# Optimization experiments

Measured on AMD Instinct MI355X. Metric: run time of the kernel, lower is better.

The kernel has to match this reference:

```python
import jax, jax.numpy as jnp
import numpy as np

N, E, B = 30000, 360000, 8
FN, FE, D, L, M = 64, 16, 128, 3, 8
DK = D // M
NEG_SLOPE = 0.2
EPS = 1e-5


def setup_inputs() -> dict:
    key = jax.random.key(0)
    ks = jax.random.split(key, 24)
    rng = np.random.default_rng(0)
    Ng, Eg = N // B, E // B
    off = np.repeat(np.arange(B, dtype=np.int64) * Ng, Eg)
    src = jnp.asarray(rng.integers(0, Ng, size=E) + off, dtype=jnp.int32)
    dst = jnp.asarray(rng.integers(0, Ng, size=E) + off, dtype=jnp.int32)
    node_graph = jnp.asarray(np.repeat(np.arange(B), Ng), dtype=jnp.int32)
    edge_graph = jnp.asarray(np.repeat(np.arange(B), Eg), dtype=jnp.int32)
    p = lambda i, *s: jax.random.normal(ks[i], s, jnp.float32) * 0.05
    return dict(
        h=jax.random.normal(ks[0], (N, FN), jnp.float32),
        e=jax.random.normal(ks[1], (E, FE), jnp.float32),
        src=src, dst=dst, node_graph=node_graph, edge_graph=edge_graph,
        emb_n_w=p(2, D, FN), emb_n_b=p(3, D),
        emb_e_w=p(4, D, FE), emb_e_b=p(5, D),
        Us=p(6, L, D, D), Vs=p(7, L, D, D), As=p(8, L, D, D),
        Bs=p(9, L, D, D), Cs=p(10, L, D, D),
        gat_src_w=p(11, M * DK, D), gat_src_b=p(12, M * DK),
        gat_dst_w=p(13, M * DK, D), gat_dst_b=p(14, M * DK),
        gat_attn=p(15, M, DK), gat_bias=p(16, M * DK),
        O_w=p(17, D, D), O_b=p(18, D),
        W1_w=p(19, D, 3 * D), W1_b=p(20, D),
        W2_w=p(21, 1, D), W2_b=p(22, 1))


def _bn(x):
    # BatchNorm1d(affine=False), training mode: biased variance over batch dim
    return (x - x.mean(0)) * jax.lax.rsqrt(x.var(0) + EPS)


def reference(h, e, src, dst, node_graph, edge_graph,
              emb_n_w, emb_n_b, emb_e_w, emb_e_b,
              Us, Vs, As, Bs, Cs,
              gat_src_w, gat_src_b, gat_dst_w, gat_dst_b, gat_attn, gat_bias,
              O_w, O_b, W1_w, W1_b, W2_w, W2_b):
    h = h @ emb_n_w.T + emb_n_b  # [N, D]
    e = e @ emb_e_w.T + emb_e_b  # [E, D]
    for l in range(L):
        # u_mul_e('h','w','m') + max('m','agg'): gather-mul-segment_max
        m = (h @ Vs[l].T)[src] * jax.nn.sigmoid(e)  # [E, D]
        agg = jax.ops.segment_max(m, dst, num_segments=N)
        agg = jnp.where(jnp.isneginf(agg), 0.0, agg)  # DGL fills zero-in-degree with 0
        h_new = h + jax.nn.relu(_bn(h @ Us[l].T + agg))
        # inc('in')^T @ B(h) = B(h)[dst]; inc('out')^T @ C(h) = C(h)[src] (uses pre-update h)
        ee = (h @ Bs[l].T)[dst] + (h @ Cs[l].T)[src]
        e = e + jax.nn.relu(_bn(e @ As[l].T + ee))
        h = h_new
    # GATv2Conv(D, DK, M heads, allow_zero_in_degree=True)
    fs = (h @ gat_src_w.T + gat_src_b).reshape(N, M, DK)
    fd = (h @ gat_dst_w.T + gat_dst_b).reshape(N, M, DK)
    z = jax.nn.leaky_relu(fs[src] + fd[dst], NEG_SLOPE)  # [E, M, DK]
    score = jnp.einsum('emk,mk->em', z, gat_attn)        # [E, M]
    smax = jax.ops.segment_max(score, dst, num_segments=N)[dst]
    p = jnp.exp(score - smax)
    denom = jax.ops.segment_sum(p, dst, num_segments=N)[dst]
    a = p / denom
    rst = jax.ops.segment_sum(a[:, :, None] * fs[src], dst, num_segments=N)
    rst = rst + gat_bias.reshape(1, M, DK)
    h = rst.reshape(N, D) @ O_w.T + O_b
    # per-graph mean of node states, broadcast to that graph's edges
    cnt = jax.ops.segment_sum(jnp.ones((N,), h.dtype), node_graph, num_segments=B)
    moy = jax.ops.segment_sum(h, node_graph, num_segments=B) / cnt[:, None]
    out = jnp.concatenate([moy[edge_graph], h[src], h[dst]], axis=1)  # [E, 3D]
    out = jax.nn.relu(out @ W1_w.T + W1_b)
    out = out @ W2_w.T + W2_b
    return jax.nn.sigmoid(out)[:, 0]
```

## Files before the change

kernel.cpp:

```cpp
#include <hip/hip_runtime.h>

#define DF 128
#define NGRAPH 8

typedef __attribute__((ext_vector_type(8))) short bf16x8;
typedef __attribute__((ext_vector_type(4))) float f32x4;

__device__ __forceinline__ float sigm(float x) { return 1.f / (1.f + __expf(-x)); }
__device__ __forceinline__ unsigned short f2bf(float f) {
  unsigned u = __float_as_uint(f);
  u += 0x7FFFu + ((u >> 16) & 1u);
  return (unsigned short)(u >> 16);
}
__device__ __forceinline__ float bf2f(unsigned short u) {
  return __uint_as_float(((unsigned)u) << 16);
}
__device__ __forceinline__ float bflo(unsigned u) { return __uint_as_float(u << 16); }
__device__ __forceinline__ float bfhi(unsigned u) { return __uint_as_float(u & 0xffff0000u); }

__device__ __forceinline__ bf16x8 cvt8(const float* __restrict__ p) {
  float4 a = *(const float4*)p;
  float4 b = *(const float4*)(p + 4);
  bf16x8 r;
  r[0] = (short)f2bf(a.x); r[1] = (short)f2bf(a.y);
// ... 119 lines not shown
  for (int i = tid; i < 16 * DF; i += 128) Wt[(i & 15) * DF + (i >> 4)] = w[i];
  float bb = b[tid];
  __syncthreads();
  for (int r0 = blockIdx.x * 4; r0 < rows; r0 += gridDim.x * 4) {
    if (tid < 64) ar[tid >> 4][tid & 15] = ein[(size_t)r0 * 16 + tid];
    __syncthreads();
    float a0 = bb, a1 = bb, a2 = bb, a3 = bb;
#pragma unroll
    for (int k = 0; k < 16; ++k) {
      float wv = Wt[k * DF + tid];
      a0 = fmaf(ar[0][k], wv, a0); a1 = fmaf(ar[1][k], wv, a1);
      a2 = fmaf(ar[2][k], wv, a2); a3 = fmaf(ar[3][k], wv, a3);
    }
    e0u[(size_t)r0 * DF + tid] = f2bf(a0);
    e0u[(size_t)(r0 + 1) * DF + tid] = f2bf(a1);
    e0u[(size_t)(r0 + 2) * DF + tid] = f2bf(a2);
    e0u[(size_t)(r0 + 3) * DF + tid] = f2bf(a3);
    __syncthreads();
  }
}

template <int OUTBF>
__global__ __launch_bounds__(512) void k_gemm_mfma(
    const float* __restrict__ A, const short* __restrict__ Wf,
    const float* __restrict__ bias, void* __restrict__ outv, int rows) {
  __shared__ short Wb[2048 * 8];
  int tid = threadIdx.x;
  for (int s = tid; s < 2048; s += 512)
    *(bf16x8*)&Wb[s * 8] = *(const bf16x8*)&Wf[(size_t)s * 8];
  __syncthreads();
  float* outf = (float*)outv;
  unsigned short* outb = (unsigned short*)outv;
  int wid = tid >> 6, lane = tid & 63, q = lane >> 4, m = lane & 15;
  int ntiles = (rows + 127) >> 7;
  for (int t = blockIdx.x; t < ntiles; t += gridDim.x) {
    int r0 = t * 128 + wid * 16;
    int rr = r0 + m;
    if (rr >= rows) rr = rows - 1;
    const float* ap = A + (size_t)rr * DF + q * 8;
    bf16x8 a[4];
#pragma unroll
    for (int ks = 0; ks < 4; ++ks) a[ks] = cvt8(ap + 32 * ks);
#pragma unroll
    for (int ct = 0; ct < 8; ++ct) {
      f32x4 acc = {0.f, 0.f, 0.f, 0.f};
#pragma unroll
      for (int ks = 0; ks < 4; ++ks) {
        bf16x8 b = *(const bf16x8*)&Wb[((ct * 4 + ks) * 64 + lane) * 8];
        acc = __builtin_amdgcn_mfma_f32_16x16x32_bf16(a[ks], b, acc, 0, 0, 0);
      }
      int col = ct * 16 + m;
      float bb = bias ? bias[col] : 0.f;
#pragma unroll
      for (int j = 0; j < 4; ++j) {
        int row = r0 + q * 4 + j;
        if (row < rows) {
          if (OUTBF) outb[(size_t)row * DF + col] = f2bf(acc[j] + bb);
          else outf[(size_t)row * DF + col] = acc[j] + bb;
        }
      }
    }
  }
}

__global__ __launch_bounds__(512) void k_gemmb_mfma(
    const unsigned short* __restrict__ A, const short* __restrict__ Wf,
    unsigned short* __restrict__ outb, int rows) {
  __shared__ short Wb[2048 * 8];
  int tid = threadIdx.x;
  for (int s = tid; s < 2048; s += 512)
    *(bf16x8*)&Wb[s * 8] = *(const bf16x8*)&Wf[(size_t)s * 8];
  __syncthreads();
  int wid = tid >> 6, lane = tid & 63, q = lane >> 4, m = lane & 15;
  int ntiles = (rows + 127) >> 7;
  for (int t = blockIdx.x; t < ntiles; t += gridDim.x) {
    int r0 = t * 128 + wid * 16;
    int rr = r0 + m;
    if (rr >= rows) rr = rows - 1;
    const unsigned short* ap = A + (size_t)rr * DF + q * 8;
    bf16x8 a[4];
#pragma unroll
    for (int ks = 0; ks < 4; ++ks) a[ks] = *(const bf16x8*)(ap + 32 * ks);
#pragma unroll
    for (int ct = 0; ct < 8; ++ct) {
      f32x4 acc = {0.f, 0.f, 0.f, 0.f};
#pragma unroll
      for (int ks = 0; ks < 4; ++ks) {
        bf16x8 b = *(const bf16x8*)&Wb[((ct * 4 + ks) * 64 + lane) * 8];
        acc = __builtin_amdgcn_mfma_f32_16x16x32_bf16(a[ks], b, acc, 0, 0, 0);
      }
      int col = ct * 16 + m;
#pragma unroll
      for (int j = 0; j < 4; ++j) {
        int row = r0 + q * 4 + j;
        if (row < rows) outb[(size_t)row * DF + col] = f2bf(acc[j]);
      }
    }
  }
}

__global__ __launch_bounds__(512) void k_gemm4_mfma(
    const float* __restrict__ h0, const short* __restrict__ Vf,
    const short* __restrict__ Uf, const short* __restrict__ Bf,
    const short* __restrict__ Cf, unsigned short* __restrict__ hVb,
    float* __restrict__ hU, unsigned short* __restrict__ hBb,
    unsigned short* __restrict__ hCb, int rows) {
  __shared__ short Wl[4 * 2048 * 8];
  int tid = threadIdx.x;
  for (int s = tid; s < 2048; s += 512) {
    *(bf16x8*)&Wl[(size_t)s * 8] = *(const bf16x8*)&Vf[(size_t)s * 8];
    *(bf16x8*)&Wl[(size_t)(2048 + s) * 8] = *(const bf16x8*)&Uf[(size_t)s * 8];
    *(bf16x8*)&Wl[(size_t)(4096 + s) * 8] = *(const bf16x8*)&Bf[(size_t)s * 8];
    *(bf16x8*)&Wl[(size_t)(6144 + s) * 8] = *(const bf16x8*)&Cf[(size_t)s * 8];
  }
  __syncthreads();
  int wid = tid >> 6, lane = tid & 63, q = lane >> 4, m = lane & 15;
  int ntiles = (rows + 127) >> 7;
  for (int t = blockIdx.x; t < ntiles; t += gridDim.x) {
    int r0 = t * 128 + wid * 16;
    int rr = r0 + m;
    if (rr >= rows) rr = rows - 1;
    const float* ap = h0 + (size_t)rr * DF + q * 8;
    bf16x8 a[4];
#pragma unroll
    for (int ks = 0; ks < 4; ++ks) a[ks] = cvt8(ap + 32 * ks);
#pragma unroll
    for (int w = 0; w < 4; ++w) {
#pragma unroll
      for (int ct = 0; ct < 8; ++ct) {
        f32x4 acc = {0.f, 0.f, 0.f, 0.f};
#pragma unroll
        for (int ks = 0; ks < 4; ++ks) {
          bf16x8 b = *(const bf16x8*)&Wl[((w * 2048) + (ct * 4 + ks) * 64 + lane) * 8];
          acc = __builtin_amdgcn_mfma_f32_16x16x32_bf16(a[ks], b, acc, 0, 0, 0);
        }
        int col = ct * 16 + m;
#pragma unroll
        for (int j = 0; j < 4; ++j) {
          int row = r0 + q * 4 + j;
          if (row < rows) {
            if (w == 1) hU[(size_t)row * DF + col] = acc[j];
            else {
              unsigned short v = f2bf(acc[j]);
              unsigned short* o = (w == 0) ? hVb : ((w == 2) ? hBb : hCb);
              o[(size_t)row * DF + col] = v;
            }
          }
        }
      }
    }
  }
}

template <int MODE>
__global__ __launch_bounds__(512) void k_edge_mfma(
    unsigned short* __restrict__ e0u, const short* __restrict__ Af,
    const unsigned short* __restrict__ hBb, const unsigned short* __restrict__ hCb,
    const int* __restrict__ src, const int* __restrict__ dst,
    float* __restrict__ stat, unsigned short* __restrict__ xe, int Eg) {
  __shared__ short Wb[2048 * 8];
  __shared__ float xt[8][16 * 132];
  int tid = threadIdx.x;
  for (int s = tid; s < 2048; s += 512)
    *(bf16x8*)&Wb[s * 8] = *(const bf16x8*)&Af[(size_t)s * 8];
  int wid = tid >> 6, lane = tid & 63, q = lane >> 4, m = lane & 15;
  int g = blockIdx.x & 7, sub = blockIdx.x >> 3, nsub = gridDim.x >> 3;
  int gbase = g * Eg, gend = gbase + Eg;
  int tpg = (Eg + 127) >> 7;
  float* xw = xt[wid];
  float ps0 = 0.f, ps1 = 0.f, pq0 = 0.f, pq1 = 0.f;
  __syncthreads();
  for (int t = sub; t < tpg; t += nsub) {
    int r0 = gbase + t * 128 + wid * 16;
    int edge = r0 + m;
    bool ok = edge < gend;
    int ec = ok ? edge : gend - 1;
    const unsigned short* ep = e0u + (size_t)ec * DF + q * 8;
    bf16x8 a[4];
#pragma unroll
    for (int ks = 0; ks < 4; ++ks) a[ks] = *(const bf16x8*)(ep + 32 * ks);
#pragma unroll
    for (int ct = 0; ct < 8; ++ct) {
      f32x4 acc = {0.f, 0.f, 0.f, 0.f};
#pragma unroll
      for (int ks = 0; ks < 4; ++ks) {
        bf16x8 b = *(const bf16x8*)&Wb[((ct * 4 + ks) * 64 + lane) * 8];
        acc = __builtin_amdgcn_mfma_f32_16x16x32_bf16(a[ks], b, acc, 0, 0, 0);
      }
#pragma unroll
      for (int j = 0; j < 4; ++j) xw[(q * 4 + j) * 132 + ct * 16 + m] = acc[j];
    }
    __syncthreads();
    int sidx = src[ec], didx = dst[ec];
    const unsigned short* pb = hBb + (size_t)didx * DF;
    const unsigned short* pc = hCb + (size_t)sidx * DF;
#pragma unroll
    for (int ks = 0; ks < 4; ++ks) {
      int c0 = q * 8 + 32 * ks;
      float* xp = &xw[m * 132 + c0];
      bf16x8 gb = *(const bf16x8*)(pb + c0);
      bf16x8 gc = *(const bf16x8*)(pc + c0);
      float x[8];
#pragma unroll
      for (int i = 0; i < 8; ++i)
        x[i] = xp[i] + bf2f((unsigned short)gb[i]) + bf2f((unsigned short)gc[i]);
      if (MODE == 1) {
        bf16x8 nv;
#pragma unroll
        for (int i = 0; i < 8; ++i) {
          float mm = stat[768 + c0 + i], iv = stat[896 + c0 + i];
          nv[i] = (short)f2bf(bf2f((unsigned short)a[ks][i]) + fmaxf((x[i] - mm) * iv, 0.f));
        }
        if (ok) *(bf16x8*)(e0u + (size_t)ec * DF + c0) = nv;
      } else {
        if (MODE == 2 && ok) {
          bf16x8 xv;
#pragma unroll
          for (int i = 0; i < 8; ++i) xv[i] = (short)f2bf(x[i]);
          *(bf16x8*)(xe + (size_t)ec * DF + c0) = xv;
        }
#pragma unroll
        for (int i = 0; i < 8; ++i) xp[i] = ok ? x[i] : 0.f;
      }
    }
    if (MODE != 1) {
      __syncthreads();
#pragma unroll 4
      for (int r = 0; r < 16; ++r) {
        float2 v = *(float2*)&xw[r * 132 + 2 * lane];
        ps0 += v.x; ps1 += v.y;
        pq0 += v.x * v.x; pq1 += v.y * v.y;
      }
    }
    __syncthreads();
  }
  if (MODE != 1) {
    atomicAdd(&stat[512 + 2 * lane], ps0);
    atomicAdd(&stat[512 + 2 * lane + 1], ps1);
    atomicAdd(&stat[640 + 2 * lane], pq0);
    atomicAdd(&stat[640 + 2 * lane + 1], pq1);
  }
}

__global__ __launch_bounds__(256) void k_edge_apply(
    unsigned short* __restrict__ e0u, const unsigned short* __restrict__ xe,
    const float* __restrict__ stat, long long n8) {
  long long i = (long long)blockIdx.x * blockDim.x + threadIdx.x;
  long long st = (long long)gridDim.x * blockDim.x;
  for (; i < n8; i += st) {
    int c0 = (int)(i & 15) * 8;
    bf16x8 ev = *(const bf16x8*)(e0u + i * 8);
    bf16x8 xv = *(const bf16x8*)(xe + i * 8);
    bf16x8 nv;
#pragma unroll
    for (int k = 0; k < 8; ++k) {
      float mm = stat[768 + c0 + k], iv = stat[896 + c0 + k];
      nv[k] = (short)f2bf(bf2f((unsigned short)ev[k]) +
                          fmaxf((bf2f((unsigned short)xv[k]) - mm) * iv, 0.f));
    }
    *(bf16x8*)(e0u + i * 8) = nv;
  }
}

__global__ __launch_bounds__(256) void k_node_agg(
    float* __restrict__ hU, const unsigned short* __restrict__ hVb,
    const unsigned short* __restrict__ e0u, const int* __restrict__ src,
    const unsigned* __restrict__ rowptr, const int* __restrict__ eidb,
    float* __restrict__ stat, int Ngr) {
  __shared__ float sr[4][256];
  int tid = threadIdx.x, wid = tid >> 6, lane = tid & 63;
  int g = blockIdx.x & 7, sub = blockIdx.x >> 3, nsub = gridDim.x >> 3;
  float ps0 = 0.f, ps1 = 0.f, pq0 = 0.f, pq1 = 0.f;
  for (int nn = sub * 4 + wid; nn < Ngr; nn += nsub * 4) {
    int n = g * Ngr + nn;
    unsigned r0 = rowptr[n], r1 = rowptr[n + 1];
    float m0 = -3.4e38f, m1 = -3.4e38f;
    for (unsigned rc = r0; rc < r1; rc += 64) {
      int batch = (int)min(64u, r1 - rc);
      int myE = eidb[rc + ((lane < batch) ? lane : 0)];
      int myS = src[myE];
      int j = 0;
      for (; j + 4 <= batch; j += 4) {
        int e0 = __shfl(myE, j, 64), e1 = __shfl(myE, j + 1, 64);
        int e2 = __shfl(myE, j + 2, 64), e3 = __shfl(myE, j + 3, 64);
        int s0 = __shfl(myS, j, 64), s1 = __shfl(myS, j + 1, 64);
        int s2 = __shfl(myS, j + 2, 64), s3 = __shfl(myS, j + 3, 64);
        unsigned h0v = *(const unsigned*)&hVb[(size_t)s0 * DF + 2 * lane];
        unsigned h1v = *(const unsigned*)&hVb[(size_t)s1 * DF + 2 * lane];
        unsigned h2v = *(const unsigned*)&hVb[(size_t)s2 * DF + 2 * lane];
        unsigned h3v = *(const unsigned*)&hVb[(size_t)s3 * DF + 2 * lane];
        unsigned v0 = *(const unsigned*)&e0u[(size_t)e0 * DF + 2 * lane];
        unsigned v1 = *(const unsigned*)&e0u[(size_t)e1 * DF + 2 * lane];
        unsigned v2 = *(const unsigned*)&e0u[(size_t)e2 * DF + 2 * lane];
        unsigned v3 = *(const unsigned*)&e0u[(size_t)e3 * DF + 2 * lane];
        agg_max(h0v, v0, m0, m1);
        agg_max(h1v, v1, m0, m1);
        agg_max(h2v, v2, m0, m1);
        agg_max(h3v, v3, m0, m1);
      }
      for (; j < batch; ++j) {
        int e = __shfl(myE, j, 64);
        int s = __shfl(myS, j, 64);
        unsigned hv = *(const unsigned*)&hVb[(size_t)s * DF + 2 * lane];
        unsigned ev = *(const unsigned*)&e0u[(size_t)e * DF + 2 * lane];
        agg_max(hv, ev, m0, m1);
      }
    }
    if (r1 == r0) { m0 = 0.f; m1 = 0.f; }
    size_t idx = (size_t)n * DF + 2 * lane;
    float2 hu = *(float2*)&hU[idx];
    float t0 = hu.x + m0, t1 = hu.y + m1;
    hu.x = t0; hu.y = t1;
    *(float2*)&hU[idx] = hu;
    ps0 += t0; ps1 += t1;
    pq0 += t0 * t0; pq1 += t1 * t1;
  }
  sr[0][tid] = ps0; sr[1][tid] = ps1; sr[2][tid] = pq0; sr[3][tid] = pq1;
  __syncthreads();
  if (tid < 64) {
    float a0 = 0.f, a1 = 0.f, b0 = 0.f, b1 = 0.f;
#pragma unroll
    for (int w = 0; w < 4; ++w) {
      a0 += sr[0][w * 64 + tid]; a1 += sr[1][w * 64 + tid];
      b0 += sr[2][w * 64 + tid]; b1 += sr[3][w * 64 + tid];
    }
    atomicAdd(&stat[2 * tid], a0);
    atomicAdd(&stat[2 * tid + 1], a1);
    atomicAdd(&stat[128 + 2 * tid], b0);
    atomicAdd(&stat[128 + 2 * tid + 1], b1);
  }
}

__global__ void k_bn_finalize(float* __restrict__ stat, float nN, float nE) {
  int tid = threadIdx.x;
  if (tid < 128) {
    float mean = stat[tid] / nN;
    float var = stat[128 + tid] / nN - mean * mean;
    stat[256 + tid] = mean;
    stat[384 + tid] = rsqrtf(fmaxf(var, 0.f) + 1e-5f);
  } else {
    int d = tid - 128;
    float mean = stat[512 + d] / nE;
    float var = stat[640 + d] / nE - mean * mean;
    stat[768 + d] = mean;
    stat[896 + d] = rsqrtf(fmaxf(var, 0.f) + 1e-5f);
  }
}

__global__ __launch_bounds__(256) void k_node_update(
    float* __restrict__ h0, const float* __restrict__ hU,
    const float* __restrict__ stat, long long total) {
  long long i = (long long)blockIdx.x * blockDim.x + threadIdx.x;
  long long st = (long long)gridDim.x * blockDim.x;
  for (; i < total; i += st) {
    int d = (int)(i & 127);
    float t = (hU[i] - stat[256 + d]) * stat[384 + d];
    h0[i] += fmaxf(t, 0.f);
  }
}

__global__ __launch_bounds__(256) void k_gat_score(
    const unsigned short* __restrict__ fsb, const unsigned short* __restrict__ fdb,
    const int* __restrict__ src, const int* __restrict__ dst,
    const float* __restrict__ attn, float* __restrict__ score, int Eg) {
  int g = blockIdx.x & 7, sub = blockIdx.x >> 3, nsub = gridDim.x >> 3;
  int gbase = g * Eg, gend = gbase + Eg;
  int tpg = (Eg + 127) >> 7;
  int tid = threadIdx.x;
  for (int t = sub; t < tpg; t += nsub) {
    int ebase = gbase + t * 128;
    for (int k = tid; k < 1024; k += 256) {
      int e = ebase + (k >> 3);
      if (e >= gend) break;
      int mh = k & 7;
      int s = src[e], dn = dst[e];
      const unsigned short* ps = fsb + (size_t)s * DF + mh * 16;
      const unsigned short* pd = fdb + (size_t)dn * DF + mh * 16;
      const float* pa = attn + mh * 16;
      bf16x8 s0 = *(const bf16x8*)ps;
      bf16x8 s1 = *(const bf16x8*)(ps + 8);
      bf16x8 d0 = *(const bf16x8*)pd;
      bf16x8 d1 = *(const bf16x8*)(pd + 8);
      float acc = 0.f;
#pragma unroll
      for (int kk = 0; kk < 8; ++kk) {
        float z = bf2f((unsigned short)s0[kk]) + bf2f((unsigned short)d0[kk]);
        z = (z > 0.f) ? z : 0.2f * z;
        acc = fmaf(z, pa[kk], acc);
        float z2 = bf2f((unsigned short)s1[kk]) + bf2f((unsigned short)d1[kk]);
        z2 = (z2 > 0.f) ? z2 : 0.2f * z2;
        acc = fmaf(z2, pa[kk + 8], acc);
      }
      score[(size_t)e * 8 + mh] = acc;
    }
  }
}

__global__ __launch_bounds__(256) void k_gat_node(
    const float* __restrict__ score, const unsigned short* __restrict__ fsb,
    const int* __restrict__ src, const unsigned* __restrict__ rowptr,
    const int* __restrict__ eidb, float* __restrict__ rst, int Ngr) {
  int tid = threadIdx.x, wid = tid >> 6, lane = tid & 63;
  int g = blockIdx.x & 7, sub = blockIdx.x >> 3, nsub = gridDim.x >> 3;
  int head = lane >> 3, slot = lane & 7;
  for (int nn = sub * 4 + wid; nn < Ngr; nn += nsub * 4) {
    int n = g * Ngr + nn;
    unsigned r0 = rowptr[n], r1 = rowptr[n + 1];
    float hm = -3.4e38f;
    for (unsigned rc = r0; rc < r1; rc += 64) {
      int batch = (int)min(64u, r1 - rc);
      int myE = eidb[rc + ((lane < batch) ? lane : 0)];
      for (int k = slot; k < batch; k += 8) {
        int e = __shfl(myE, k, 64);
// ... 56 lines not shown
}

__global__ void k_bias2(const float* __restrict__ gat_bias,
                        const float* __restrict__ O_w,
                        const float* __restrict__ O_b, float* __restrict__ bias2) {
  int d = threadIdx.x;
  float acc = O_b[d];
  for (int k = 0; k < DF; ++k) acc = fmaf(gat_bias[k], O_w[(size_t)d * DF + k], acc);
  bias2[d] = acc;
}

__global__ __launch_bounds__(128) void k_moy(
    const unsigned short* __restrict__ h2b, const int* __restrict__ ng,
    float* __restrict__ moy, float* __restrict__ cnt, int rows) {
  int tid = threadIdx.x;
  int per = (rows + gridDim.x - 1) / gridDim.x;
  int n0 = blockIdx.x * per;
  int n1 = min(rows, n0 + per);
  if (n0 >= n1) return;
  int cur = ng[n0];
  float acc = 0.f; int c = 0;
  for (int n = n0; n < n1; ++n) {
    int g = ng[n];
    if (g != cur) {
      atomicAdd(&moy[cur * DF + tid], acc);
      if (tid == 0) atomicAdd(&cnt[cur], (float)c);
      acc = 0.f; c = 0; cur = g;
    }
    acc += bf2f(h2b[(size_t)n * DF + tid]);
    ++c;
  }
  atomicAdd(&moy[cur * DF + tid], acc);
  if (tid == 0) atomicAdd(&cnt[cur], (float)c);
}

__global__ void k_p0(const float* __restrict__ W1, const float* __restrict__ W1b_,
                     const float* __restrict__ moy, const float* __restrict__ cnt,
                     float* __restrict__ P0) {
  int g = blockIdx.x, d = threadIdx.x;
  float inv = 1.f / cnt[g];
  float acc = W1b_[d];
  for (int k = 0; k < DF; ++k) acc = fmaf(W1[(size_t)d * 384 + k], moy[g * DF + k] * inv, acc);
  P0[g * DF + d] = acc;
}

__global__ __launch_bounds__(256) void k_head(
    const unsigned short* __restrict__ P1b, const unsigned short* __restrict__ P2b,
    const float* __restrict__ P0, const int* __restrict__ src,
    const unsigned* __restrict__ rowptr, const int* __restrict__ eidb,
    const float* __restrict__ W2, const float* __restrict__ W2b,
    float* __restrict__ out, int Ngr) {
  int tid = threadIdx.x, wid = tid >> 6, lane = tid & 63;
  int g = blockIdx.x & 7, sub = blockIdx.x >> 3, nsub = gridDim.x >> 3;
  float w2b = W2b[0];
  float w20 = W2[2 * lane], w21 = W2[2 * lane + 1];
  float b0 = P0[g * DF + 2 * lane], b1v = P0[g * DF + 2 * lane + 1];
  for (int nn = sub * 4 + wid; nn < Ngr; nn += nsub * 4) {
    int n = g * Ngr + nn;
    unsigned r0 = rowptr[n], r1 = rowptr[n + 1];
    if (r1 == r0) continue;
    unsigned p2 = *(const unsigned*)&P2b[(size_t)n * DF + 2 * lane];
    float base0 = b0 + bflo(p2);
    float base1 = b1v + bfhi(p2);
    for (unsigned rc = r0; rc < r1; rc += 64) {
      int cnt2 = (int)min(64u, r1 - rc);
      int myE = eidb[rc + ((lane < cnt2) ? lane : 0)];
      int myS = src[myE];
      int j = 0;
      for (; j + 4 <= cnt2; j += 4) {
        int e0 = __shfl(myE, j, 64), e1 = __shfl(myE, j + 1, 64);
        int e2 = __shfl(myE, j + 2, 64), e3 = __shfl(myE, j + 3, 64);
        int s0 = __shfl(myS, j, 64), s1 = __shfl(myS, j + 1, 64);
        int s2 = __shfl(myS, j + 2, 64), s3 = __shfl(myS, j + 3, 64);
        unsigned u0 = *(const unsigned*)&P1b[(size_t)s0 * DF + 2 * lane];
        unsigned u1 = *(const unsigned*)&P1b[(size_t)s1 * DF + 2 * lane];
        unsigned u2 = *(const unsigned*)&P1b[(size_t)s2 * DF + 2 * lane];
        unsigned u3 = *(const unsigned*)&P1b[(size_t)s3 * DF + 2 * lane];
        float v0 = fmaxf(base0 + bflo(u0), 0.f) * w20 + fmaxf(base1 + bfhi(u0), 0.f) * w21;
        float v1 = fmaxf(base0 + bflo(u1), 0.f) * w20 + fmaxf(base1 + bfhi(u1), 0.f) * w21;
        float v2 = fmaxf(base0 + bflo(u2), 0.f) * w20 + fmaxf(base1 + bfhi(u2), 0.f) * w21;
        float v3 = fmaxf(base0 + bflo(u3), 0.f) * w20 + fmaxf(base1 + bfhi(u3), 0.f) * w21;
#pragma unroll
        for (int mk = 1; mk < 64; mk <<= 1) {
          v0 += __shfl_xor(v0, mk, 64);
          v1 += __shfl_xor(v1, mk, 64);
          v2 += __shfl_xor(v2, mk, 64);
          v3 += __shfl_xor(v3, mk, 64);
        }
        if (lane == 0) {
          out[e0] = sigm(v0 + w2b);
          out[e1] = sigm(v1 + w2b);
          out[e2] = sigm(v2 + w2b);
          out[e3] = sigm(v3 + w2b);
        }
      }
      for (; j < cnt2; ++j) {
        int e = __shfl(myE, j, 64);
        int s = __shfl(myS, j, 64);
        unsigned p1 = *(const unsigned*)&P1b[(size_t)s * DF + 2 * lane];
        float v = fmaxf(base0 + bflo(p1), 0.f) * w20 + fmaxf(base1 + bfhi(p1), 0.f) * w21;
#pragma unroll
        for (int mk = 1; mk < 64; mk <<= 1) v += __shfl_xor(v, mk, 64);
        if (lane == 0) out[e] = sigm(v + w2b);
      }
    }
  }
}

extern "C" void kernel_launch(void* const* d_in, const int* in_sizes, int n_in,
                              void* d_out, int out_size, void* d_ws, size_t ws_size,
                              hipStream_t stream) {
  const float* h_in = (const float*)d_in[0];
  const float* e_in = (const float*)d_in[1];
  const int* src = (const int*)d_in[2];
  const int* dst = (const int*)d_in[3];
  const int* node_graph = (const int*)d_in[4];
  const float* emb_n_w = (const float*)d_in[6];
  const float* emb_n_b = (const float*)d_in[7];
  const float* emb_e_w = (const float*)d_in[8];
  const float* emb_e_b = (const float*)d_in[9];
  const float* Us = (const float*)d_in[10];
  const float* Vs = (const float*)d_in[11];
  const float* As = (const float*)d_in[12];
  const float* Bs = (const float*)d_in[13];
  const float* Cs = (const float*)d_in[14];
  const float* gat_src_w = (const float*)d_in[15];
  const float* gat_src_b = (const float*)d_in[16];
  const float* gat_dst_w = (const float*)d_in[17];
  const float* gat_dst_b = (const float*)d_in[18];
  const float* gat_attn = (const float*)d_in[19];
  const float* gat_bias = (const float*)d_in[20];
  const float* O_w = (const float*)d_in[21];
  const float* O_b = (const float*)d_in[22];
  const float* W1_w = (const float*)d_in[23];
  const float* W1_b = (const float*)d_in[24];
  const float* W2_w = (const float*)d_in[25];
  const float* W2_b = (const float*)d_in[26];
  float* out = (float*)d_out;

  const int N = in_sizes[0] / 64;
  const int E = in_sizes[1] / 16;
  const int Eg = E / NGRAPH;
  const int Ngr = N / NGRAPH;

  auto rnd = [](size_t b) { return (b + 255) & ~(size_t)255; };
  const size_t sz_e0 = rnd((size_t)E * DF * 2);
  const size_t sz_node = rnd((size_t)N * DF * 4);
  const size_t sz_nodeb = rnd((size_t)N * DF * 2);
  const size_t sz_score = rnd((size_t)E * 8 * 4);
  const size_t sz_wfrag = rnd(20 * 2048 * 8 * 2);
  const size_t sz_rp = rnd((size_t)(N + 1) * 4);
  const size_t sz_eid = rnd((size_t)E * 4);
  const size_t sz_misc = rnd(4096 * 4);
  const size_t needed_min = sz_e0 + 3 * sz_node + 4 * sz_nodeb + sz_score + sz_wfrag +
                            3 * sz_rp + sz_eid + sz_misc;
  const size_t needed_full = needed_min + sz_e0;
  if (ws_size < needed_min) {
    k_fill_u32<<<256, 256, 0, stream>>>((unsigned*)out, 0xBF800000u, (long long)out_size);
    return;
  }
  const bool have_xe = (ws_size >= needed_full);

  char* wp = (char*)d_ws;
  auto alloc = [&](size_t bytes) { void* p = wp; wp += bytes; return p; };
  unsigned short* e0u = (unsigned short*)alloc(sz_e0);
  float* h0 = (float*)alloc(sz_node);
  float* hU = (float*)alloc(sz_node);
  float* rst = (float*)alloc(sz_node);
  unsigned short* hVb = (unsigned short*)alloc(sz_nodeb);
  unsigned short* hBb = (unsigned short*)alloc(sz_nodeb);
  unsigned short* hCb = (unsigned short*)alloc(sz_nodeb);
  unsigned short* h2b = (unsigned short*)alloc(sz_nodeb);
  float* score = (float*)alloc(sz_score);
  short* wfrag = (short*)alloc(sz_wfrag);
  unsigned* rowptr = (unsigned*)alloc(sz_rp);
  unsigned* cursor = (unsigned*)alloc(sz_rp);
  unsigned* deg = (unsigned*)alloc(sz_rp);
  int* eidb = (int*)alloc(sz_eid);
  float* misc = (float*)alloc(sz_misc);
  unsigned short* xe = have_xe ? (unsigned short*)alloc(sz_e0) : nullptr;
  float* stat = misc;
  float* bias2 = misc + 1024;
  float* moy = misc + 1152;
  float* cnt = misc + 2176;
  float* P0 = misc + 2304;
  unsigned short* P1b = e0u;
  unsigned short* P2b = e0u + (size_t)N * DF;

  auto WF = [&](int idx) { return wfrag + (size_t)idx * 2048 * 8; };

  k_fill_u32<<<64, 256, 0, stream>>>(deg, 0u, N);
  k_deg<<<512, 256, 0, stream>>>(dst, deg, E);
  k_scan<<<1, 1024, 0, stream>>>(deg, rowptr, cursor, N);
  k_scatter<<<512, 256, 0, stream>>>(dst, cursor, eidb, E);

  k_wconv<<<20, 512, 0, stream>>>(Us, Vs, As, Bs, Cs, gat_src_w, gat_dst_w, O_w,
                                  W1_w, wfrag);

  const int gN = (N + 127) / 128;
  k_node_embed<<<2048, 128, 0, stream>>>(h_in, emb_n_w, emb_n_b, h0, N);
  k_edge_embed<<<4096, 128, 0, stream>>>(e_in, emb_e_w, emb_e_b, e0u, E);

  for (int l = 0; l < 3; ++l) {
    k_gemm4_mfma<<<gN, 512, 0, stream>>>(h0, WF(3 + l), WF(l), WF(9 + l), WF(12 + l),
                                         hVb, hU, hBb, hCb, N);
    k_fill_u32<<<4, 256, 0, stream>>>((unsigned*)stat, 0u, 1024);
    k_node_agg<<<2048, 256, 0, stream>>>(hU, hVb, e0u, src, rowptr, eidb, stat, Ngr);
    if (have_xe) {
      k_edge_mfma<2><<<256, 512, 0, stream>>>(e0u, WF(6 + l), hBb, hCb, src, dst,
                                              stat, xe, Eg);
      k_bn_finalize<<<1, 256, 0, stream>>>(stat, (float)N, (float)E);
      k_node_update<<<2048, 256, 0, stream>>>(h0, hU, stat, (long long)N * DF);
      k_edge_apply<<<2048, 256, 0, stream>>>(e0u, xe, stat, (long long)E * DF / 8);
    } else {
      k_edge_mfma<0><<<256, 512, 0, stream>>>(e0u, WF(6 + l), hBb, hCb, src, dst,
                                              stat, nullptr, Eg);
      k_bn_finalize<<<1, 256, 0, stream>>>(stat, (float)N, (float)E);
      k_node_update<<<2048, 256, 0, stream>>>(h0, hU, stat, (long long)N * DF);
      k_edge_mfma<1><<<256, 512, 0, stream>>>(e0u, WF(6 + l), hBb, hCb, src, dst,
                                              stat, nullptr, Eg);
    }
  }

  k_gemm_mfma<1><<<gN, 512, 0, stream>>>(h0, WF(15), gat_src_b, hVb, N);
  k_gemm_mfma<1><<<gN, 512, 0, stream>>>(h0, WF(16), gat_dst_b, hBb, N);
  k_gat_score<<<512, 256, 0, stream>>>(hVb, hBb, src, dst, gat_attn, score, Eg);
  k_gat_node<<<2048, 256, 0, stream>>>(score, hVb, src, rowptr, eidb, rst, Ngr);
  k_bias2<<<1, 128, 0, stream>>>(gat_bias, O_w, O_b, bias2);
  k_gemm_mfma<1><<<gN, 512, 0, stream>>>(rst, WF(17), bias2, h2b, N);

  k_fill_u32<<<2, 256, 0, stream>>>((unsigned*)moy, 0u, 1032);
  k_moy<<<128, 128, 0, stream>>>(h2b, node_graph, moy, cnt, N);
  k_p0<<<8, 128, 0, stream>>>(W1_w, W1_b, moy, cnt, P0);
  k_gemmb_mfma<<<gN, 512, 0, stream>>>(h2b, WF(18), P1b, N);
  k_gemmb_mfma<<<gN, 512, 0, stream>>>(h2b, WF(19), P2b, N);
  k_head<<<2048, 256, 0, stream>>>(P1b, P2b, P0, src, rowptr, eidb, W2_w, W2_b,
                                   out, Ngr);
}
```

Measured before the change: 1.478 ms.

## Split edge GEMM from BatchNorm statistics into separate streaming kernels

Replaces the fused edge MFMA kernel (mode 2) with a lean kernel that computes the edge pre-activation and writes it directly in bf16 from MFMA accumulators, without LDS staging or per-tile barriers. Column sums and squared sums for BatchNorm are then computed by a separate streaming reduction over the stored tensor. This is meant to remove LDS transpose and synchronisation overhead and to raise occupancy in the GEMM pass. The cost is an extra full read of the edge pre-activation tensor for every layer.

```diff
diff --git a/kernel.cpp b/kernel.cpp
--- a/kernel.cpp
+++ b/kernel.cpp
@@ -295,12 +295,103 @@
   }
 }
 
+__global__ __launch_bounds__(512) void k_edge_x(
+    const unsigned short* __restrict__ e0u, const short* __restrict__ Af,
+    const unsigned short* __restrict__ hBb, const unsigned short* __restrict__ hCb,
+    const int* __restrict__ src, const int* __restrict__ dst,
+    unsigned short* __restrict__ xe, int Eg) {
+  __shared__ short Wb[2048 * 8];
+  int tid = threadIdx.x;
+  for (int s = tid; s < 2048; s += 512)
+    *(bf16x8*)&Wb[s * 8] = *(const bf16x8*)&Af[(size_t)s * 8];
+  __syncthreads();
+  int wid = tid >> 6, lane = tid & 63, q = lane >> 4, m = lane & 15;
+  int g = blockIdx.x & 7, sub = blockIdx.x >> 3, nsub = gridDim.x >> 3;
+  int gbase = g * Eg, gend = gbase + Eg;
+  int tpg = (Eg + 127) >> 7;
+  for (int t = sub; t < tpg; t += nsub) {
+    int r0 = gbase + t * 128 + wid * 16;
+    int edge = r0 + m;
+    bool ok = edge < gend;
+    int ec = ok ? edge : gend - 1;
+    const unsigned short* ep = e0u + (size_t)ec * DF + q * 8;
+    bf16x8 b[4];
+#pragma unroll
+    for (int ks = 0; ks < 4; ++ks) b[ks] = *(const bf16x8*)(ep + 32 * ks);
+    f32x4 c0 = {0.f, 0.f, 0.f, 0.f}, c1 = c0, c2 = c0, c3 = c0;
+    f32x4 c4 = c0, c5 = c0, c6 = c0, c7 = c0;
+#pragma unroll
+    for (int ks = 0; ks < 4; ++ks) {
+      bf16x8 bv = b[ks];
+      c0 = __builtin_amdgcn_mfma_f32_16x16x32_bf16(*(const bf16x8*)&Wb[((0 * 4 + ks) * 64 + lane) * 8], bv, c0, 0, 0, 0);
+      c1 = __builtin_amdgcn_mfma_f32_16x16x32_bf16(*(const bf16x8*)&Wb[((1 * 4 + ks) * 64 + lane) * 8], bv, c1, 0, 0, 0);
+      c2 = __builtin_amdgcn_mfma_f32_16x16x32_bf16(*(const bf16x8*)&Wb[((2 * 4 + ks) * 64 + lane) * 8], bv, c2, 0, 0, 0);
+      c3 = __builtin_amdgcn_mfma_f32_16x16x32_bf16(*(const bf16x8*)&Wb[((3 * 4 + ks) * 64 + lane) * 8], bv, c3, 0, 0, 0);
+      c4 = __builtin_amdgcn_mfma_f32_16x16x32_bf16(*(const bf16x8*)&Wb[((4 * 4 + ks) * 64 + lane) * 8], bv, c4, 0, 0, 0);
+      c5 = __builtin_amdgcn_mfma_f32_16x16x32_bf16(*(const bf16x8*)&Wb[((5 * 4 + ks) * 64 + lane) * 8], bv, c5, 0, 0, 0);
+      c6 = __builtin_amdgcn_mfma_f32_16x16x32_bf16(*(const bf16x8*)&Wb[((6 * 4 + ks) * 64 + lane) * 8], bv, c6, 0, 0, 0);
+      c7 = __builtin_amdgcn_mfma_f32_16x16x32_bf16(*(const bf16x8*)&Wb[((7 * 4 + ks) * 64 + lane) * 8], bv, c7, 0, 0, 0);
+    }
+    if (ok) {
+      int sidx = src[ec], didx = dst[ec];
+      const unsigned short* pb = hBb + (size_t)didx * DF + q * 4;
+      const unsigned short* pc = hCb + (size_t)sidx * DF + q * 4;
+      unsigned short* px = xe + (size_t)ec * DF + q * 4;
+#pragma unroll
+      for (int ct = 0; ct < 8; ++ct) {
+        f32x4 cc = (ct == 0) ? c0 : (ct == 1) ? c1 : (ct == 2) ? c2 : (ct == 3) ? c3
+                   : (ct == 4) ? c4 : (ct == 5) ? c5 : (ct == 6) ? c6 : c7;
+        ushort4 hb = *(const ushort4*)(pb + ct * 16);
+        ushort4 hc = *(const ushort4*)(pc + ct * 16);
+        ushort4 xv;
+        xv.x = f2bf(cc[0] + bf2f(hb.x) + bf2f(hc.x));
+        xv.y = f2bf(cc[1] + bf2f(hb.y) + bf2f(hc.y));
+        xv.z = f2bf(cc[2] + bf2f(hb.z) + bf2f(hc.z));
+        xv.w = f2bf(cc[3] + bf2f(hb.w) + bf2f(hc.w));
+        *(ushort4*)(px + ct * 16) = xv;
+      }
+    }
+  }
+}
+
+__global__ __launch_bounds__(256) void k_xstats(
+    const unsigned short* __restrict__ xe, float* __restrict__ stat, long long n8) {
+  __shared__ float ls[256];
+  int tid = threadIdx.x;
+  ls[tid] = 0.f;
+  __syncthreads();
+  float ps[8] = {0.f, 0.f, 0.f, 0.f, 0.f, 0.f, 0.f, 0.f};
+  float pq[8] = {0.f, 0.f, 0.f, 0.f, 0.f, 0.f, 0.f, 0.f};
+  long long i = (long long)blockIdx.x * 256 + tid;
+  long long st = (long long)gridDim.x * 256;
+  for (; i < n8; i += st) {
+    bf16x8 v = *(const bf16x8*)(xe + i * 8);
+#pragma unroll
+    for (int k = 0; k < 8; ++k) {
+      float f = bf2f((unsigned short)v[k]);
+      ps[k] += f;
+      pq[k] += f * f;
+    }
+  }
+  int c0 = (tid & 15) * 8;
+#pragma unroll
+  for (int k = 0; k < 8; ++k) {
+    atomicAdd(&ls[c0 + k], ps[k]);
+    atomicAdd(&ls[128 + c0 + k], pq[k]);
+  }
+  __syncthreads();
+  if (tid < 128) {
+    atomicAdd(&stat[512 + tid], ls[tid]);
+    atomicAdd(&stat[640 + tid], ls[128 + tid]);
+  }
+}
+
 template <int MODE>
 __global__ __launch_bounds__(512) void k_edge_mfma(
     unsigned short* __restrict__ e0u, const short* __restrict__ Af,
     const unsigned short* __restrict__ hBb, const unsigned short* __restrict__ hCb,
     const int* __restrict__ src, const int* __restrict__ dst,
-    float* __restrict__ stat, unsigned short* __restrict__ xe, int Eg) {
+    float* __restrict__ stat, int Eg) {
   __shared__ short Wb[2048 * 8];
   __shared__ float xt[8][16 * 132];
   int tid = threadIdx.x;
@@ -356,12 +447,6 @@
         }
         if (ok) *(bf16x8*)(e0u + (size_t)ec * DF + c0) = nv;
       } else {
-        if (MODE == 2 && ok) {
-          bf16x8 xv;
-#pragma unroll
-          for (int i = 0; i < 8; ++i) xv[i] = (short)f2bf(x[i]);
-          *(bf16x8*)(xe + (size_t)ec * DF + c0) = xv;
-        }
 #pragma unroll
         for (int i = 0; i < 8; ++i) xp[i] = ok ? x[i] : 0.f;
       }
@@ -819,18 +904,18 @@
     k_fill_u32<<<4, 256, 0, stream>>>((unsigned*)stat, 0u, 1024);
     k_node_agg<<<2048, 256, 0, stream>>>(hU, hVb, e0u, src, rowptr, eidb, stat, Ngr);
     if (have_xe) {
-      k_edge_mfma<2><<<256, 512, 0, stream>>>(e0u, WF(6 + l), hBb, hCb, src, dst,
-                                              stat, xe, Eg);
+      k_edge_x<<<512, 512, 0, stream>>>(e0u, WF(6 + l), hBb, hCb, src, dst, xe, Eg);
+      k_xstats<<<512, 256, 0, stream>>>(xe, stat, (long long)E * DF / 8);
       k_bn_finalize<<<1, 256, 0, stream>>>(stat, (float)N, (float)E);
       k_node_update<<<2048, 256, 0, stream>>>(h0, hU, stat, (long long)N * DF);
       k_edge_apply<<<2048, 256, 0, stream>>>(e0u, xe, stat, (long long)E * DF / 8);
     } else {
       k_edge_mfma<0><<<256, 512, 0, stream>>>(e0u, WF(6 + l), hBb, hCb, src, dst,
-                                              stat, nullptr, Eg);
+                                              stat, Eg);
       k_bn_finalize<<<1, 256, 0, stream>>>(stat, (float)N, (float)E);
       k_node_update<<<2048, 256, 0, stream>>>(h0, hU, stat, (long long)N * DF);
       k_edge_mfma<1><<<256, 512, 0, stream>>>(e0u, WF(6 + l), hBb, hCb, src, dst,
-                                              stat, nullptr, Eg);
+                                              stat, Eg);
     }
   }
 
```

Result: no change. 1.477 ms (-0.0%).

## Recompute edge GEMM in two passes with register-resident accumulators, drop xe buffer

Applied to the files above, without the earlier changes.

Replaces the old edge path, which stored the pre-BN edge activation to an xe buffer and then ran a separate apply kernel, with two kernels that both recompute the edge GEMM. The first accumulates BN statistics directly from MFMA accumulator registers, reduced with wave shuffles and LDS atomics. The second applies normalization in place. The GEMM is transposed so each lane holds per-feature outputs, which removes the LDS staging tile and the block barriers. Grid size goes from 256 to 1024 blocks. This trades the xe write and read traffic for a duplicated GEMM and a second read of e0u, and raises register pressure from the 32-element stat arrays.

```diff
diff --git a/kernel.cpp b/kernel.cpp
--- a/kernel.cpp
+++ b/kernel.cpp
@@ -295,113 +295,146 @@
   }
 }
 
-template <int MODE>
-__global__ __launch_bounds__(512) void k_edge_mfma(
-    unsigned short* __restrict__ e0u, const short* __restrict__ Af,
+
+#define EDGE_MFMA_BODY                                                                 \
+  const unsigned short* ep = e0u + (size_t)ec * DF + q * 8;                            \
+  bf16x8 bv0 = *(const bf16x8*)(ep);                                                   \
+  bf16x8 bv1 = *(const bf16x8*)(ep + 32);                                              \
+  bf16x8 bv2 = *(const bf16x8*)(ep + 64);                                              \
+  bf16x8 bv3 = *(const bf16x8*)(ep + 96);                                              \
+  f32x4 c0 = {0.f, 0.f, 0.f, 0.f}, c1 = c0, c2 = c0, c3 = c0;                          \
+  f32x4 c4 = c0, c5 = c0, c6 = c0, c7 = c0;                                            \
+  _Pragma("unroll") for (int ks = 0; ks < 4; ++ks) {                                   \
+    bf16x8 bv = (ks == 0) ? bv0 : (ks == 1) ? bv1 : (ks == 2) ? bv2 : bv3;             \
+    c0 = __builtin_amdgcn_mfma_f32_16x16x32_bf16(*(const bf16x8*)&Wb[((0 * 4 + ks) * 64 + lane) * 8], bv, c0, 0, 0, 0); \
+    c1 = __builtin_amdgcn_mfma_f32_16x16x32_bf16(*(const bf16x8*)&Wb[((1 * 4 + ks) * 64 + lane) * 8], bv, c1, 0, 0, 0); \
+    c2 = __builtin_amdgcn_mfma_f32_16x16x32_bf16(*(const bf16x8*)&Wb[((2 * 4 + ks) * 64 + lane) * 8], bv, c2, 0, 0, 0); \
+    c3 = __builtin_amdgcn_mfma_f32_16x16x32_bf16(*(const bf16x8*)&Wb[((3 * 4 + ks) * 64 + lane) * 8], bv, c3, 0, 0, 0); \
+    c4 = __builtin_amdgcn_mfma_f32_16x16x32_bf16(*(const bf16x8*)&Wb[((4 * 4 + ks) * 64 + lane) * 8], bv, c4, 0, 0, 0); \
+    c5 = __builtin_amdgcn_mfma_f32_16x16x32_bf16(*(const bf16x8*)&Wb[((5 * 4 + ks) * 64 + lane) * 8], bv, c5, 0, 0, 0); \
+    c6 = __builtin_amdgcn_mfma_f32_16x16x32_bf16(*(const bf16x8*)&Wb[((6 * 4 + ks) * 64 + lane) * 8], bv, c6, 0, 0, 0); \
+    c7 = __builtin_amdgcn_mfma_f32_16x16x32_bf16(*(const bf16x8*)&Wb[((7 * 4 + ks) * 64 + lane) * 8], bv, c7, 0, 0, 0); \
+  }
+
+__global__ __launch_bounds__(512) void k_edge_xs(
+    const unsigned short* __restrict__ e0u, const short* __restrict__ Af,
     const unsigned short* __restrict__ hBb, const unsigned short* __restrict__ hCb,
     const int* __restrict__ src, const int* __restrict__ dst,
-    float* __restrict__ stat, unsigned short* __restrict__ xe, int Eg) {
+    float* __restrict__ stat, int Eg) {
   __shared__ short Wb[2048 * 8];
-  __shared__ float xt[8][16 * 132];
+  __shared__ float ls[256];
   int tid = threadIdx.x;
   for (int s = tid; s < 2048; s += 512)
     *(bf16x8*)&Wb[s * 8] = *(const bf16x8*)&Af[(size_t)s * 8];
+  if (tid < 256) ls[tid] = 0.f;
   int wid = tid >> 6, lane = tid & 63, q = lane >> 4, m = lane & 15;
   int g = blockIdx.x & 7, sub = blockIdx.x >> 3, nsub = gridDim.x >> 3;
   int gbase = g * Eg, gend = gbase + Eg;
   int tpg = (Eg + 127) >> 7;
-  float* xw = xt[wid];
-  float ps0 = 0.f, ps1 = 0.f, pq0 = 0.f, pq1 = 0.f;
+  float ps[32], pq[32];
+#pragma unroll
+  for (int i = 0; i < 32; ++i) { ps[i] = 0.f; pq[i] = 0.f; }
   __syncthreads();
   for (int t = sub; t < tpg; t += nsub) {
     int r0 = gbase + t * 128 + wid * 16;
     int edge = r0 + m;
     bool ok = edge < gend;
     int ec = ok ? edge : gend - 1;
-    const unsigned short* ep = e0u + (size_t)ec * DF + q * 8;
-    bf16x8 a[4];
-#pragma unroll
-    for (int ks = 0; ks < 4; ++ks) a[ks] = *(const bf16x8*)(ep + 32 * ks);
-#pragma unroll
-    for (int ct = 0; ct < 8; ++ct) {
-      f32x4 acc = {0.f, 0.f, 0.f, 0.f};
-#pragma unroll
-      for (int ks = 0; ks < 4; ++ks) {
-        bf16x8 b = *(const bf16x8*)&Wb[((ct * 4 + ks) * 64 + lane) * 8];
-        acc = __builtin_amdgcn_mfma_f32_16x16x32_bf16(a[ks], b, acc, 0, 0, 0);
-      }
-#pragma unroll
-      for (int j = 0; j < 4; ++j) xw[(q * 4 + j) * 132 + ct * 16 + m] = acc[j];
-    }
-    __syncthreads();
-    int sidx = src[ec], didx = dst[ec];
-    const unsigned short* pb = hBb + (size_t)didx * DF;
-    const unsigned short* pc = hCb + (size_t)sidx * DF;
-#pragma unroll
-    for (int ks = 0; ks < 4; ++ks) {
-      int c0 = q * 8 + 32 * ks;
-      float* xp = &xw[m * 132 + c0];
-      bf16x8 gb = *(const bf16x8*)(pb + c0);
-      bf16x8 gc = *(const bf16x8*)(pc + c0);
-      float x[8];
-#pragma unroll
-      for (int i = 0; i < 8; ++i)
-        x[i] = xp[i] + bf2f((unsigned short)gb[i]) + bf2f((unsigned short)gc[i]);
-      if (MODE == 1) {
-        bf16x8 nv;
-#pragma unroll
-        for (int i = 0; i < 8; ++i) {
-          float mm = stat[768 + c0 + i], iv = stat[896 + c0 + i];
-          nv[i] = (short)f2bf(bf2f((unsigned short)a[ks][i]) + fmaxf((x[i] - mm) * iv, 0.f));
-        }
-        if (ok) *(bf16x8*)(e0u + (size_t)ec * DF + c0) = nv;
-      } else {
-        if (MODE == 2 && ok) {
-          bf16x8 xv;
-#pragma unroll
-          for (int i = 0; i < 8; ++i) xv[i] = (short)f2bf(x[i]);
-          *(bf16x8*)(xe + (size_t)ec * DF + c0) = xv;
-        }
-#pragma unroll
-        for (int i = 0; i < 8; ++i) xp[i] = ok ? x[i] : 0.f;
-      }
-    }
-    if (MODE != 1) {
-      __syncthreads();
-#pragma unroll 4
-      for (int r = 0; r < 16; ++r) {
-        float2 v = *(float2*)&xw[r * 132 + 2 * lane];
-        ps0 += v.x; ps1 += v.y;
-        pq0 += v.x * v.x; pq1 += v.y * v.y;
-      }
-    }
-    __syncthreads();
-  }
-  if (MODE != 1) {
-    atomicAdd(&stat[512 + 2 * lane], ps0);
-    atomicAdd(&stat[512 + 2 * lane + 1], ps1);
-    atomicAdd(&stat[640 + 2 * lane], pq0);
-    atomicAdd(&stat[640 + 2 * lane + 1], pq1);
-  }
-}
-
-__global__ __launch_bounds__(256) void k_edge_apply(
-    unsigned short* __restrict__ e0u, const unsigned short* __restrict__ xe,
-    const float* __restrict__ stat, long long n8) {
-  long long i = (long long)blockIdx.x * blockDim.x + threadIdx.x;
-  long long st = (long long)gridDim.x * blockDim.x;
-  for (; i < n8; i += st) {
-    int c0 = (int)(i & 15) * 8;
-    bf16x8 ev = *(const bf16x8*)(e0u + i * 8);
-    bf16x8 xv = *(const bf16x8*)(xe + i * 8);
-    bf16x8 nv;
-#pragma unroll
-    for (int k = 0; k < 8; ++k) {
-      float mm = stat[768 + c0 + k], iv = stat[896 + c0 + k];
-      nv[k] = (short)f2bf(bf2f((unsigned short)ev[k]) +
-                          fmaxf((bf2f((unsigned short)xv[k]) - mm) * iv, 0.f));
-    }
-    *(bf16x8*)(e0u + i * 8) = nv;
+    EDGE_MFMA_BODY
+    if (ok) {
+      int sidx = src[ec], didx = dst[ec];
+      const unsigned short* pb = hBb + (size_t)didx * DF + q * 4;
+      const unsigned short* pc = hCb + (size_t)sidx * DF + q * 4;
+#pragma unroll
+      for (int ct = 0; ct < 8; ++ct) {
+        f32x4 cc = (ct == 0) ? c0 : (ct == 1) ? c1 : (ct == 2) ? c2 : (ct == 3) ? c3
+                   : (ct == 4) ? c4 : (ct == 5) ? c5 : (ct == 6) ? c6 : c7;
+        ushort4 hb = *(const ushort4*)(pb + ct * 16);
+        ushort4 hc = *(const ushort4*)(pc + ct * 16);
+        float x0 = cc[0] + bf2f(hb.x) + bf2f(hc.x);
+        float x1 = cc[1] + bf2f(hb.y) + bf2f(hc.y);
+        float x2 = cc[2] + bf2f(hb.z) + bf2f(hc.z);
+        float x3 = cc[3] + bf2f(hb.w) + bf2f(hc.w);
+        ps[ct * 4 + 0] += x0; pq[ct * 4 + 0] += x0 * x0;
+        ps[ct * 4 + 1] += x1; pq[ct * 4 + 1] += x1 * x1;
+        ps[ct * 4 + 2] += x2; pq[ct * 4 + 2] += x2 * x2;
+        ps[ct * 4 + 3] += x3; pq[ct * 4 + 3] += x3 * x3;
+      }
+    }
+  }
+#pragma unroll
+  for (int i = 0; i < 32; ++i) {
+    float s = ps[i], sq = pq[i];
+    s += __shfl_xor(s, 1, 64); sq += __shfl_xor(sq, 1, 64);
+    s += __shfl_xor(s, 2, 64); sq += __shfl_xor(sq, 2, 64);
+    s += __shfl_xor(s, 4, 64); sq += __shfl_xor(sq, 4, 64);
+    s += __shfl_xor(s, 8, 64); sq += __shfl_xor(sq, 8, 64);
+    if (m == 0) {
+      int feat = (i >> 2) * 16 + q * 4 + (i & 3);
+      atomicAdd(&ls[feat], s);
+      atomicAdd(&ls[128 + feat], sq);
+    }
+  }
+  __syncthreads();
+  if (tid < 128) {
+    atomicAdd(&stat[512 + tid], ls[tid]);
+    atomicAdd(&stat[640 + tid], ls[128 + tid]);
+  }
+}
+
+__global__ __launch_bounds__(512) void k_edge_xa(
+    unsigned short* __restrict__ e0u, const short* __restrict__ Af,
+    const unsigned short* __restrict__ hBb, const unsigned short* __restrict__ hCb,
+    const int* __restrict__ src, const int* __restrict__ dst,
+    const float* __restrict__ stat, int Eg) {
+  __shared__ short Wb[2048 * 8];
+  int tid = threadIdx.x;
+  for (int s = tid; s < 2048; s += 512)
+    *(bf16x8*)&Wb[s * 8] = *(const bf16x8*)&Af[(size_t)s * 8];
+  int wid = tid >> 6, lane = tid & 63, q = lane >> 4, m = lane & 15;
+  float mm[32], iv[32];
+#pragma unroll
+  for (int ct = 0; ct < 8; ++ct)
+#pragma unroll
+    for (int j = 0; j < 4; ++j) {
+      int f = ct * 16 + q * 4 + j;
+      mm[ct * 4 + j] = stat[768 + f];
+      iv[ct * 4 + j] = stat[896 + f];
+    }
+  int g = blockIdx.x & 7, sub = blockIdx.x >> 3, nsub = gridDim.x >> 3;
+  int gbase = g * Eg, gend = gbase + Eg;
+  int tpg = (Eg + 127) >> 7;
+  __syncthreads();
+  for (int t = sub; t < tpg; t += nsub) {
+    int r0 = gbase + t * 128 + wid * 16;
+    int edge = r0 + m;
+    bool ok = edge < gend;
+    int ec = ok ? edge : gend - 1;
+    EDGE_MFMA_BODY
+    if (ok) {
+      int sidx = src[ec], didx = dst[ec];
+      const unsigned short* pb = hBb + (size_t)didx * DF + q * 4;
+      const unsigned short* pc = hCb + (size_t)sidx * DF + q * 4;
+      unsigned short* pe = e0u + (size_t)ec * DF + q * 4;
+#pragma unroll
+      for (int ct = 0; ct < 8; ++ct) {
+        f32x4 cc = (ct == 0) ? c0 : (ct == 1) ? c1 : (ct == 2) ? c2 : (ct == 3) ? c3
+                   : (ct == 4) ? c4 : (ct == 5) ? c5 : (ct == 6) ? c6 : c7;
+        ushort4 hb = *(const ushort4*)(pb + ct * 16);
+        ushort4 hc = *(const ushort4*)(pc + ct * 16);
+        ushort4 eo = *(const ushort4*)(pe + ct * 16);
+        float x0 = cc[0] + bf2f(hb.x) + bf2f(hc.x);
+        float x1 = cc[1] + bf2f(hb.y) + bf2f(hc.y);
+        float x2 = cc[2] + bf2f(hb.z) + bf2f(hc.z);
+        float x3 = cc[3] + bf2f(hb.w) + bf2f(hc.w);
+        ushort4 nv;
+        nv.x = f2bf(bf2f(eo.x) + fmaxf((x0 - mm[ct * 4 + 0]) * iv[ct * 4 + 0], 0.f));
+        nv.y = f2bf(bf2f(eo.y) + fmaxf((x1 - mm[ct * 4 + 1]) * iv[ct * 4 + 1], 0.f));
+        nv.z = f2bf(bf2f(eo.z) + fmaxf((x2 - mm[ct * 4 + 2]) * iv[ct * 4 + 2], 0.f));
+        nv.w = f2bf(bf2f(eo.w) + fmaxf((x3 - mm[ct * 4 + 3]) * iv[ct * 4 + 3], 0.f));
+        *(ushort4*)(pe + ct * 16) = nv;
+      }
+    }
   }
 }
 
@@ -764,14 +797,12 @@
   const size_t sz_rp = rnd((size_t)(N + 1) * 4);
   const size_t sz_eid = rnd((size_t)E * 4);
   const size_t sz_misc = rnd(4096 * 4);
-  const size_t needed_min = sz_e0 + 3 * sz_node + 4 * sz_nodeb + sz_score + sz_wfrag +
-                            3 * sz_rp + sz_eid + sz_misc;
-  const size_t needed_full = needed_min + sz_e0;
-  if (ws_size < needed_min) {
+  const size_t needed = sz_e0 + 3 * sz_node + 4 * sz_nodeb + sz_score + sz_wfrag +
+                        3 * sz_rp + sz_eid + sz_misc;
+  if (ws_size < needed) {
     k_fill_u32<<<256, 256, 0, stream>>>((unsigned*)out, 0xBF800000u, (long long)out_size);
     return;
   }
-  const bool have_xe = (ws_size >= needed_full);
 
   char* wp = (char*)d_ws;
   auto alloc = [&](size_t bytes) { void* p = wp; wp += bytes; return p; };
@@ -790,7 +821,6 @@
   unsigned* deg = (unsigned*)alloc(sz_rp);
   int* eidb = (int*)alloc(sz_eid);
   float* misc = (float*)alloc(sz_misc);
-  unsigned short* xe = have_xe ? (unsigned short*)alloc(sz_e0) : nullptr;
   float* stat = misc;
   float* bias2 = misc + 1024;
   float* moy = misc + 1152;
@@ -818,20 +848,10 @@
                                          hVb, hU, hBb, hCb, N);
     k_fill_u32<<<4, 256, 0, stream>>>((unsigned*)stat, 0u, 1024);
     k_node_agg<<<2048, 256, 0, stream>>>(hU, hVb, e0u, src, rowptr, eidb, stat, Ngr);
-    if (have_xe) {
-      k_edge_mfma<2><<<256, 512, 0, stream>>>(e0u, WF(6 + l), hBb, hCb, src, dst,
-                                              stat, xe, Eg);
-      k_bn_finalize<<<1, 256, 0, stream>>>(stat, (float)N, (float)E);
-      k_node_update<<<2048, 256, 0, stream>>>(h0, hU, stat, (long long)N * DF);
-      k_edge_apply<<<2048, 256, 0, stream>>>(e0u, xe, stat, (long long)E * DF / 8);
-    } else {
-      k_edge_mfma<0><<<256, 512, 0, stream>>>(e0u, WF(6 + l), hBb, hCb, src, dst,
-                                              stat, nullptr, Eg);
-      k_bn_finalize<<<1, 256, 0, stream>>>(stat, (float)N, (float)E);
-      k_node_update<<<2048, 256, 0, stream>>>(h0, hU, stat, (long long)N * DF);
-      k_edge_mfma<1><<<256, 512, 0, stream>>>(e0u, WF(6 + l), hBb, hCb, src, dst,
-                                              stat, nullptr, Eg);
-    }
+    k_edge_xs<<<1024, 512, 0, stream>>>(e0u, WF(6 + l), hBb, hCb, src, dst, stat, Eg);
+    k_bn_finalize<<<1, 256, 0, stream>>>(stat, (float)N, (float)E);
+    k_node_update<<<2048, 256, 0, stream>>>(h0, hU, stat, (long long)N * DF);
+    k_edge_xa<<<1024, 512, 0, stream>>>(e0u, WF(6 + l), hBb, hCb, src, dst, stat, Eg);
   }
 
   k_gemm_mfma<1><<<gN, 512, 0, stream>>>(h0, WF(15), gat_src_b, hVb, N);
```

Result: no change. 1.473 ms (-0.3%).
